# Kernel tuning notes

Hardware: AMD Instinct MI355X
Metric: run time of the kernel (lower is better)

The kernel has to match this reference:

```python
import jax, jax.numpy as jnp
import numpy as np

B, T, C = 4, 2048, 1024
N_HEAD = 16
HEAD_DIM = C // N_HEAD

def setup_inputs() -> dict:
    key = jax.random.key(0)
    k1, k2, k3 = jax.random.split(key, 3)
    x = jax.random.normal(k1, (B, T, C), dtype=jnp.float32)
    # nn.Linear(C, 3C, bias=False): weight [3C, C], y = x @ W.T
    w_qkv = jax.random.normal(k2, (3 * C, C), dtype=jnp.float32) * (1.0 / np.sqrt(C))
    w_proj = jax.random.normal(k3, (C, C), dtype=jnp.float32) * (1.0 / np.sqrt(C))
    return {"x": x, "w_qkv": w_qkv, "w_proj": w_proj}

def reference(x, w_qkv, w_proj):
    Bx, Tx, Cx = x.shape
    qkv = x @ w_qkv.T  # [B,T,3C]
    q, k, v = jnp.split(qkv, 3, axis=-1)
    def heads(t):
        return t.reshape(Bx, Tx, N_HEAD, HEAD_DIM).transpose(0, 2, 1, 3)  # [B,H,T,D]
    q, k, v = heads(q), heads(k), heads(v)
    scale = HEAD_DIM ** -0.5
    att = jnp.einsum('bhtd,bhsd->bhts', q, k) * scale  # [B,H,T,T]
    causal = jnp.tril(jnp.ones((Tx, Tx), dtype=bool))
    att = jnp.where(causal[None, None], att, -jnp.inf)
    att = jax.nn.softmax(att, axis=-1)
    y = jnp.einsum('bhts,bhsd->bhtd', att, v)  # [B,H,T,D]
    y = y.transpose(0, 2, 1, 3).reshape(Bx, Tx, Cx)
    return y @ w_proj.T
```

## Files before the change

kernel.cpp:

```cpp
#include <hip/hip_runtime.h>
#include <hip/hip_bf16.h>

typedef __attribute__((ext_vector_type(8))) short bf16x8;
typedef __attribute__((ext_vector_type(4))) float f32x4;
typedef __attribute__((ext_vector_type(4))) unsigned short ushort4v;

__device__ __forceinline__ unsigned short f2bf(float f) {
  union { float f; unsigned u; } v; v.f = f;
  unsigned r = v.u + 0x7FFFu + ((v.u >> 16) & 1u);
  return (unsigned short)(r >> 16);
}

__device__ __forceinline__ void gll16(const void* g, void* l) {
  __builtin_amdgcn_global_load_lds((const __attribute__((address_space(1))) void*)g,
                                   (__attribute__((address_space(3))) void*)l, 16, 0, 0);
}

#define MFMA16(a, b, c) __builtin_amdgcn_mfma_f32_16x16x32_bf16((a), (b), (c), 0, 0, 0)

__global__ void cvt_f32_bf16(const float* __restrict__ s, unsigned short* __restrict__ d, int n) {
  int i = (blockIdx.x * blockDim.x + threadIdx.x) * 4;
  if (i >= n) return;
  float4 f = *(const float4*)(s + i);
  ushort4v r;
  r[0] = f2bf(f.x); r[1] = f2bf(f.y); r[2] = f2bf(f.z); r[3] = f2bf(f.w);
  *(ushort4v*)(d + i) = r;
}

template<int EPI>
__global__ __launch_bounds__(256, 2)
void gemm_nt(const unsigned short* __restrict__ A,
             const unsigned short* __restrict__ B,
             unsigned short* __restrict__ obf,
             float* __restrict__ of32,
             int M, int N, int K) {
  __shared__ unsigned short At[128 * 64];
  __shared__ unsigned short Bt[128 * 64];
  const int tid = threadIdx.x, wid = tid >> 6, lane = tid & 63;
  const int c = lane & 15, g = lane >> 4;
  const int wr = wid >> 1, wc = wid & 1;
  const int m0 = blockIdx.x * 128, n0 = blockIdx.y * 128;

  f32x4 acc[4][4];
#pragma unroll
  for (int i = 0; i < 4; ++i)
#pragma unroll
    for (int j = 0; j < 4; ++j) acc[i][j] = f32x4{0.f, 0.f, 0.f, 0.f};

  for (int kt = 0; kt < K; kt += 64) {
    if (kt) __syncthreads();
#pragma unroll
    for (int r = 0; r < 4; ++r) {
      int chunk = wid * 4 + r;
      int row = chunk * 8 + (lane >> 3);
      int col = (lane & 7) * 8;
      gll16(A + (size_t)(m0 + row) * K + kt + col, At + chunk * 512);
      gll16(B + (size_t)(n0 + row) * K + kt + col, Bt + chunk * 512);
    }
    __syncthreads();
#pragma unroll
    for (int kk = 0; kk < 2; ++kk) {
      bf16x8 af[4], bfr[4];
#pragma unroll
      for (int i = 0; i < 4; ++i) {
        af[i]  = *(const bf16x8*)(At + (wr * 64 + i * 16 + c) * 64 + kk * 32 + g * 8);
        bfr[i] = *(const bf16x8*)(Bt + (wc * 64 + i * 16 + c) * 64 + kk * 32 + g * 8);
      }
#pragma unroll
      for (int mi = 0; mi < 4; ++mi)
#pragma unroll
        for (int ni = 0; ni < 4; ++ni)
          acc[mi][ni] = MFMA16(af[mi], bfr[ni], acc[mi][ni]);
    }
  }

#pragma unroll
  for (int mi = 0; mi < 4; ++mi)
#pragma unroll
    for (int ni = 0; ni < 4; ++ni)
#pragma unroll
      for (int r4 = 0; r4 < 4; ++r4) {
        float v = acc[mi][ni][r4];
        int mg = m0 + wr * 64 + mi * 16 + g * 4 + r4;
        int ng = n0 + wc * 64 + ni * 16 + c;
        if (EPI == 0) {
          int which = ng >> 10, rem = ng & 1023;
          int hh = rem >> 6, dd = rem & 63;
          int bb = mg >> 11, tt = mg & 2047;
          size_t idx = (size_t)which * 8388608u + ((size_t)(bb * 16 + hh) * 2048 + tt) * 64 + dd;
          obf[idx] = f2bf(v);
        } else {
          of32[(size_t)mg * N + ng] = v;
        }
      }
}

__global__ __launch_bounds__(256, 2)
void attn_fwd(const unsigned short* __restrict__ qb,
              const unsigned short* __restrict__ kb,
              const unsigned short* __restrict__ vb,
              unsigned short* __restrict__ yb) {
  __shared__ unsigned short Kt[64 * 64];
  __shared__ unsigned short Vt[64 * 64];
  __shared__ unsigned short Pl[4 * 16 * 64];
  const int tid = threadIdx.x, w = tid >> 6, lane = tid & 63;
  const int c = lane & 15, g = lane >> 4;
  const int bh = blockIdx.x & 63;
  const int qt = 31 - (blockIdx.x >> 6);
  const int q0 = qt * 64;
  const int b = bh >> 4, h = bh & 15;
  const size_t hb = (size_t)bh * 131072;

  const unsigned short* qp = qb + hb + (size_t)(q0 + w * 16 + c) * 64;
  bf16x8 qf[2];
  qf[0] = *(const bf16x8*)(qp + g * 8);
  qf[1] = *(const bf16x8*)(qp + 32 + g * 8);

  f32x4 yacc[4];
#pragma unroll
  for (int i = 0; i < 4; ++i) yacc[i] = f32x4{0.f, 0.f, 0.f, 0.f};
  float mrun[4] = {-1e30f, -1e30f, -1e30f, -1e30f};
  float lsum[4] = {0.f, 0.f, 0.f, 0.f};
  unsigned short* pw = Pl + w * 1024;

  for (int kv = 0; kv <= qt; ++kv) {
    const int kv0 = kv * 64;
    if (kv) __syncthreads();
#pragma unroll
    for (int r = 0; r < 2; ++r) {
      int chunk = w * 2 + r;
      int row = chunk * 8 + (lane >> 3);
      int bo = (lane & 7) * 16;
      int sbo = bo ^ ((row & 7) << 4);
      gll16((const char*)(kb + hb + (size_t)(kv0 + row) * 64) + sbo, Kt + chunk * 512);
    }
    {
      const unsigned short* vp = vb + hb + (size_t)(kv0 + lane) * 64 + w * 16;
      bf16x8 v0 = *(const bf16x8*)(vp);
      bf16x8 v1 = *(const bf16x8*)(vp + 8);
#pragma unroll
      for (int i = 0; i < 8; ++i) {
        int d0 = w * 16 + i;
        Vt[d0 * 64 + (lane ^ ((d0 & 7) << 3))] = (unsigned short)v0[i];
        int d1 = w * 16 + 8 + i;
        Vt[d1 * 64 + (lane ^ ((d1 & 7) << 3))] = (unsigned short)v1[i];
      }
    }
    __syncthreads();

    f32x4 sacc[4];
#pragma unroll
    for (int nt = 0; nt < 4; ++nt) sacc[nt] = f32x4{0.f, 0.f, 0.f, 0.f};
#pragma unroll
    for (int kk = 0; kk < 2; ++kk)
#pragma unroll
      for (int nt = 0; nt < 4; ++nt) {
        int row = nt * 16 + c;
        bf16x8 kf = *(const bf16x8*)(Kt + row * 64 + ((kk * 32 + g * 8) ^ ((row & 7) << 3)));
        sacc[nt] = MFMA16(qf[kk], kf, sacc[nt]);
      }

    float mt[4];
#pragma unroll
    for (int r4 = 0; r4 < 4; ++r4) {
      int qrow = q0 + w * 16 + g * 4 + r4;
      float mx = -1e30f;
#pragma unroll
      for (int nt = 0; nt < 4; ++nt) {
        int col = kv0 + nt * 16 + c;
        float s = sacc[nt][r4] * 0.125f;
        s = (col <= qrow) ? s : -1e30f;
        sacc[nt][r4] = s;
        mx = fmaxf(mx, s);
      }
      mt[r4] = mx;
    }
#pragma unroll
    for (int off = 1; off < 16; off <<= 1)
#pragma unroll
      for (int r4 = 0; r4 < 4; ++r4) mt[r4] = fmaxf(mt[r4], __shfl_xor(mt[r4], off));

#pragma unroll
    for (int r4 = 0; r4 < 4; ++r4) {
      float mnew = fmaxf(mrun[r4], mt[r4]);
      float corr = __expf(mrun[r4] - mnew);
      mrun[r4] = mnew;
      float psum = 0.f;
      int prow = g * 4 + r4;
#pragma unroll
      for (int nt = 0; nt < 4; ++nt) {
        float p = __expf(sacc[nt][r4] - mnew);
        psum += p;
        pw[prow * 64 + ((nt * 16 + c) ^ ((prow & 7) << 3))] = f2bf(p);
      }
      lsum[r4] = lsum[r4] * corr + psum;
#pragma unroll
      for (int dt = 0; dt < 4; ++dt) yacc[dt][r4] *= corr;
    }

#pragma unroll
    for (int kk = 0; kk < 2; ++kk) {
      bf16x8 pa = *(const bf16x8*)(pw + c * 64 + ((kk * 32 + g * 8) ^ ((c & 7) << 3)));
#pragma unroll
      for (int dt = 0; dt < 4; ++dt) {
        int n = dt * 16 + c;
        bf16x8 vf = *(const bf16x8*)(Vt + n * 64 + ((kk * 32 + g * 8) ^ ((n & 7) << 3)));
        yacc[dt] = MFMA16(pa, vf, yacc[dt]);
      }
    }
  }

#pragma unroll
  for (int off = 1; off < 16; off <<= 1)
#pragma unroll
    for (int r4 = 0; r4 < 4; ++r4) lsum[r4] += __shfl_xor(lsum[r4], off);
#pragma unroll
  for (int dt = 0; dt < 4; ++dt)
#pragma unroll
    for (int r4 = 0; r4 < 4; ++r4) {
      int row = q0 + w * 16 + g * 4 + r4;
      float yv = yacc[dt][r4] / lsum[r4];
      yb[((size_t)(b * 2048 + row)) * 1024 + h * 64 + dt * 16 + c] = f2bf(yv);
    }
}

extern "C" void kernel_launch(void* const* d_in, const int* in_sizes, int n_in,
                              void* d_out, int out_size, void* d_ws, size_t ws_size,
                              hipStream_t stream) {
  const float* x     = (const float*)d_in[0];
  const float* wqkv  = (const float*)d_in[1];
  const float* wproj = (const float*)d_in[2];
  float* out = (float*)d_out;

  unsigned short* ws     = (unsigned short*)d_ws;
  unsigned short* xb     = ws;
  unsigned short* wqkvb  = xb + 8388608;
  unsigned short* wprojb = wqkvb + 3145728;
  unsigned short* qkvb   = wprojb + 1048576;
  unsigned short* yb     = qkvb + 3 * 8388608;

  cvt_f32_bf16<<<8192, 256, 0, stream>>>(x, xb, 8388608);
  cvt_f32_bf16<<<3072, 256, 0, stream>>>(wqkv, wqkvb, 3145728);
  cvt_f32_bf16<<<1024, 256, 0, stream>>>(wproj, wprojb, 1048576);

  gemm_nt<0><<<dim3(64, 24), 256, 0, stream>>>(xb, wqkvb, qkvb, nullptr, 8192, 3072, 1024);
  attn_fwd<<<2048, 256, 0, stream>>>(qkvb, qkvb + 8388608, qkvb + 2 * 8388608, yb);
  gemm_nt<1><<<dim3(64, 8), 256, 0, stream>>>(yb, wprojb, nullptr, out, 8192, 1024, 1024);
}
```

Measured before the change: 205.8 us.

## Transpose attention MFMA operands, use exp2 softmax with lazy rescale

```diff
diff --git a/kernel.cpp b/kernel.cpp
--- a/kernel.cpp
+++ b/kernel.cpp
@@ -4,11 +4,17 @@
 typedef __attribute__((ext_vector_type(8))) short bf16x8;
 typedef __attribute__((ext_vector_type(4))) float f32x4;
 typedef __attribute__((ext_vector_type(4))) unsigned short ushort4v;
+typedef __attribute__((ext_vector_type(2))) unsigned uint2v;
 
 __device__ __forceinline__ unsigned short f2bf(float f) {
   union { float f; unsigned u; } v; v.f = f;
   unsigned r = v.u + 0x7FFFu + ((v.u >> 16) & 1u);
   return (unsigned short)(r >> 16);
+}
+
+__device__ __forceinline__ unsigned pack_bf2(float lo, float hi) {
+  __hip_bfloat162 h = __float22bfloat162_rn(make_float2(lo, hi));
+  union { __hip_bfloat162 h; unsigned u; } cv; cv.h = h; return cv.u;
 }
 
 __device__ __forceinline__ void gll16(const void* g, void* l) {
@@ -95,14 +101,14 @@
       }
 }
 
-__global__ __launch_bounds__(256, 2)
+__global__ __launch_bounds__(256, 4)
 void attn_fwd(const unsigned short* __restrict__ qb,
               const unsigned short* __restrict__ kb,
               const unsigned short* __restrict__ vb,
               unsigned short* __restrict__ yb) {
   __shared__ unsigned short Kt[64 * 64];
   __shared__ unsigned short Vt[64 * 64];
-  __shared__ unsigned short Pl[4 * 16 * 64];
+  __shared__ unsigned short Pl[4 * 16 * 72];
   const int tid = threadIdx.x, w = tid >> 6, lane = tid & 63;
   const int c = lane & 15, g = lane >> 4;
   const int bh = blockIdx.x & 63;
@@ -110,21 +116,21 @@
   const int q0 = qt * 64;
   const int b = bh >> 4, h = bh & 15;
   const size_t hb = (size_t)bh * 131072;
+  const float GAM = 0.125f * 1.44269504089f;
 
   const unsigned short* qp = qb + hb + (size_t)(q0 + w * 16 + c) * 64;
-  bf16x8 qf[2];
-  qf[0] = *(const bf16x8*)(qp + g * 8);
-  qf[1] = *(const bf16x8*)(qp + 32 + g * 8);
+  bf16x8 qf0 = *(const bf16x8*)(qp + g * 8);
+  bf16x8 qf1 = *(const bf16x8*)(qp + 32 + g * 8);
 
   f32x4 yacc[4];
 #pragma unroll
   for (int i = 0; i < 4; ++i) yacc[i] = f32x4{0.f, 0.f, 0.f, 0.f};
-  float mrun[4] = {-1e30f, -1e30f, -1e30f, -1e30f};
-  float lsum[4] = {0.f, 0.f, 0.f, 0.f};
-  unsigned short* pw = Pl + w * 1024;
+  float mrun = -1e30f, lsum = 0.f;
+  unsigned short* pw = Pl + w * (16 * 72);
 
   for (int kv = 0; kv <= qt; ++kv) {
     const int kv0 = kv * 64;
+    const bool diag = (kv == qt);
     if (kv) __syncthreads();
 #pragma unroll
     for (int r = 0; r < 2; ++r) {
@@ -135,15 +141,16 @@
       gll16((const char*)(kb + hb + (size_t)(kv0 + row) * 64) + sbo, Kt + chunk * 512);
     }
     {
-      const unsigned short* vp = vb + hb + (size_t)(kv0 + lane) * 64 + w * 16;
-      bf16x8 v0 = *(const bf16x8*)(vp);
-      bf16x8 v1 = *(const bf16x8*)(vp + 8);
+      int kv2 = (lane & 31) * 2;
+      int dblk = w * 16 + (lane >> 5) * 8;
+      const unsigned short* vp = vb + hb + (size_t)(kv0 + kv2) * 64 + dblk;
+      bf16x8 r0 = *(const bf16x8*)(vp);
+      bf16x8 r1 = *(const bf16x8*)(vp + 64);
 #pragma unroll
       for (int i = 0; i < 8; ++i) {
-        int d0 = w * 16 + i;
-        Vt[d0 * 64 + (lane ^ ((d0 & 7) << 3))] = (unsigned short)v0[i];
-        int d1 = w * 16 + 8 + i;
-        Vt[d1 * 64 + (lane ^ ((d1 & 7) << 3))] = (unsigned short)v1[i];
+        int d = dblk + i;
+        unsigned pk2 = ((unsigned)(unsigned short)r0[i]) | (((unsigned)(unsigned short)r1[i]) << 16);
+        *(unsigned*)(Vt + d * 64 + (kv2 ^ ((d & 7) << 3))) = pk2;
       }
     }
     __syncthreads();
@@ -157,71 +164,76 @@
       for (int nt = 0; nt < 4; ++nt) {
         int row = nt * 16 + c;
         bf16x8 kf = *(const bf16x8*)(Kt + row * 64 + ((kk * 32 + g * 8) ^ ((row & 7) << 3)));
-        sacc[nt] = MFMA16(qf[kk], kf, sacc[nt]);
-      }
-
-    float mt[4];
-#pragma unroll
-    for (int r4 = 0; r4 < 4; ++r4) {
-      int qrow = q0 + w * 16 + g * 4 + r4;
-      float mx = -1e30f;
-#pragma unroll
-      for (int nt = 0; nt < 4; ++nt) {
-        int col = kv0 + nt * 16 + c;
-        float s = sacc[nt][r4] * 0.125f;
-        s = (col <= qrow) ? s : -1e30f;
-        sacc[nt][r4] = s;
-        mx = fmaxf(mx, s);
-      }
-      mt[r4] = mx;
-    }
-#pragma unroll
-    for (int off = 1; off < 16; off <<= 1)
-#pragma unroll
-      for (int r4 = 0; r4 < 4; ++r4) mt[r4] = fmaxf(mt[r4], __shfl_xor(mt[r4], off));
-
-#pragma unroll
-    for (int r4 = 0; r4 < 4; ++r4) {
-      float mnew = fmaxf(mrun[r4], mt[r4]);
-      float corr = __expf(mrun[r4] - mnew);
-      mrun[r4] = mnew;
-      float psum = 0.f;
-      int prow = g * 4 + r4;
-#pragma unroll
-      for (int nt = 0; nt < 4; ++nt) {
-        float p = __expf(sacc[nt][r4] - mnew);
-        psum += p;
-        pw[prow * 64 + ((nt * 16 + c) ^ ((prow & 7) << 3))] = f2bf(p);
-      }
-      lsum[r4] = lsum[r4] * corr + psum;
-#pragma unroll
-      for (int dt = 0; dt < 4; ++dt) yacc[dt][r4] *= corr;
-    }
+        sacc[nt] = MFMA16(kf, (kk ? qf1 : qf0), sacc[nt]);
+      }
+
+    if (diag) {
+      int ql = w * 16 + c;
+#pragma unroll
+      for (int nt = 0; nt < 4; ++nt)
+#pragma unroll
+        for (int r = 0; r < 4; ++r)
+          if (nt * 16 + g * 4 + r > ql) sacc[nt][r] = -1e30f;
+    }
+
+    float m0 = -1e30f;
+#pragma unroll
+    for (int nt = 0; nt < 4; ++nt) {
+      float a = fmaxf(fmaxf(sacc[nt][0], sacc[nt][1]), fmaxf(sacc[nt][2], sacc[nt][3]));
+      m0 = fmaxf(m0, a);
+    }
+    m0 = fmaxf(m0, __shfl_xor(m0, 16));
+    m0 = fmaxf(m0, __shfl_xor(m0, 32));
+
+    if (__any(m0 > mrun + 32.0f)) {
+      float mnew = fmaxf(mrun, m0);
+      float corr = __builtin_amdgcn_exp2f(GAM * (mrun - mnew));
+      lsum *= corr;
+#pragma unroll
+      for (int dt = 0; dt < 4; ++dt) yacc[dt] *= corr;
+      mrun = mnew;
+    }
+
+    float bexp = -GAM * mrun;
+    float psum = 0.f;
+#pragma unroll
+    for (int nt = 0; nt < 4; ++nt) {
+      float p0 = __builtin_amdgcn_exp2f(fmaf(sacc[nt][0], GAM, bexp));
+      float p1 = __builtin_amdgcn_exp2f(fmaf(sacc[nt][1], GAM, bexp));
+      float p2 = __builtin_amdgcn_exp2f(fmaf(sacc[nt][2], GAM, bexp));
+      float p3 = __builtin_amdgcn_exp2f(fmaf(sacc[nt][3], GAM, bexp));
+      psum += (p0 + p1) + (p2 + p3);
+      uint2v pkv;
+      pkv[0] = pack_bf2(p0, p1);
+      pkv[1] = pack_bf2(p2, p3);
+      *(uint2v*)(pw + c * 72 + nt * 16 + g * 4) = pkv;
+    }
+    lsum += psum;
 
 #pragma unroll
     for (int kk = 0; kk < 2; ++kk) {
-      bf16x8 pa = *(const bf16x8*)(pw + c * 64 + ((kk * 32 + g * 8) ^ ((c & 7) << 3)));
+      bf16x8 pb = *(const bf16x8*)(pw + c * 72 + kk * 32 + g * 8);
 #pragma unroll
       for (int dt = 0; dt < 4; ++dt) {
         int n = dt * 16 + c;
         bf16x8 vf = *(const bf16x8*)(Vt + n * 64 + ((kk * 32 + g * 8) ^ ((n & 7) << 3)));
-        yacc[dt] = MFMA16(pa, vf, yacc[dt]);
+        yacc[dt] = MFMA16(vf, pb, yacc[dt]);
       }
     }
   }
 
-#pragma unroll
-  for (int off = 1; off < 16; off <<= 1)
-#pragma unroll
-    for (int r4 = 0; r4 < 4; ++r4) lsum[r4] += __shfl_xor(lsum[r4], off);
-#pragma unroll
-  for (int dt = 0; dt < 4; ++dt)
-#pragma unroll
-    for (int r4 = 0; r4 < 4; ++r4) {
-      int row = q0 + w * 16 + g * 4 + r4;
-      float yv = yacc[dt][r4] / lsum[r4];
-      yb[((size_t)(b * 2048 + row)) * 1024 + h * 64 + dt * 16 + c] = f2bf(yv);
-    }
+  lsum += __shfl_xor(lsum, 16);
+  lsum += __shfl_xor(lsum, 32);
+  float inv = 1.0f / lsum;
+  int row = q0 + w * 16 + c;
+  unsigned short* yp = yb + ((size_t)(b * 2048 + row)) * 1024 + h * 64;
+#pragma unroll
+  for (int dt = 0; dt < 4; ++dt) {
+    uint2v pkv;
+    pkv[0] = pack_bf2(yacc[dt][0] * inv, yacc[dt][1] * inv);
+    pkv[1] = pack_bf2(yacc[dt][2] * inv, yacc[dt][3] * inv);
+    *(uint2v*)(yp + dt * 16 + g * 4) = pkv;
+  }
 }
 
 extern "C" void kernel_launch(void* const* d_in, const int* in_sizes, int n_in,
```

Result: faster. 180.4 us (-12.3%).
